# Optimization experiments

Hardware: AMD Instinct MI355X
Metric: run time of the kernel (lower is better)

The kernel has to match this reference:

```python
import jax, jax.numpy as jnp
import numpy as np

U_A = 110.0  # upper bound of feature norm (init kwarg u_a)


def setup_inputs() -> dict:
    key = jax.random.key(0)
    k1, k2, k3, k4 = jax.random.split(key, 4)
    B, C = 256, 100000
    cos_theta = jax.random.normal(k1, (B, C), dtype=jnp.float32)
    cos_theta_m = jax.random.normal(k2, (B, C), dtype=jnp.float32)
    # feature norms in [l_a, u_a] = [10, 110]
    x_norm = 10.0 + 100.0 * jax.random.uniform(k3, (B,), dtype=jnp.float32)
    target = jax.random.randint(k4, (B,), 0, C, dtype=jnp.int32)
    return {"cos_theta": cos_theta, "cos_theta_m": cos_theta_m,
            "x_norm": x_norm, "target": target}


def reference(cos_theta, cos_theta_m, x_norm, target):
    B, C = cos_theta.shape
    # one-hot scatter: one_hot[i, target[i]] = 1 (world_size=1 -> full class dim)
    one_hot = jax.nn.one_hot(target, C, dtype=cos_theta.dtype)  # [B, C]
    # loss_G regularizer: g = x_norm / u_a^2 + 1 / x_norm
    loss_g = jnp.mean(x_norm / (U_A * U_A) + 1.0 / x_norm)
    # margin blend: use cos_theta_m at the target class, cos_theta elsewhere
    output = one_hot * cos_theta_m + (1.0 - one_hot) * cos_theta  # [B, C]
    # cross-entropy with stable log-softmax (distributed LSE collapses to this)
    logp = jax.nn.log_softmax(output, axis=-1)
    loss = -jnp.take_along_axis(logp, target[:, None], axis=-1)[:, 0]  # [B]
    return (loss.mean(), loss_g, one_hot)
```

## Files before the change

kernel.cpp:

```cpp
#include <hip/hip_runtime.h>


#define UA2_INV (1.0f / 12100.0f)
#define SEG 8
#define SEG_SHIFT 3

typedef float v4f __attribute__((ext_vector_type(4)));
typedef float v2f __attribute__((ext_vector_type(2)));

__device__ __forceinline__ void fix_target(float4& v, int c, int t4, int kt4,
                                           float ctm_t) {
    if (c == t4) {
        v.x = (kt4 == 0) ? ctm_t : v.x;
        v.y = (kt4 == 1) ? ctm_t : v.y;
        v.z = (kt4 == 2) ? ctm_t : v.z;
        v.w = (kt4 == 3) ? ctm_t : v.w;
    }
}

__device__ __forceinline__ float exp_sum4(const float4& v) {
    return (__expf(v.x) + __expf(v.y)) + (__expf(v.z) + __expf(v.w));
}

__device__ __forceinline__ void do_fill(float* __restrict__ oh, int seg, int t,
                                        int C, int tid) {
    v4f* __restrict__ oh4 = (v4f*)(oh + 2);
    const int K   = (C - 2) >> 2;
    const int ups = (K + SEG - 1) >> SEG_SHIFT;
    const int u0 = seg * ups;
    const int u1 = min(u0 + ups, K);
    const int ut = (t >= 2) ? ((t - 2) >> 2) : -1;
    const int kt = (t - 2) & 3;

    for (int u = u0 + tid; u < u1; u += 256) {
        v4f z = {0.f, 0.f, 0.f, 0.f};
        if (u == ut) {
            z.x = (kt == 0) ? 1.f : 0.f;
            z.y = (kt == 1) ? 1.f : 0.f;
            z.z = (kt == 2) ? 1.f : 0.f;
            z.w = (kt == 3) ? 1.f : 0.f;
        }
        oh4[u] = z;
    }
    if (seg == 0 && tid == 1) {
        v2f f;
        f.x = (t == 0) ? 1.f : 0.f;
        f.y = (t == 1) ? 1.f : 0.f;
        *(v2f*)oh = f;
    }
    if (seg == SEG - 1) {
        for (int j = 2 + 4 * K + tid; j < C; j += 256)
            oh[j] = (j == t) ? 1.f : 0.f;
    }
}

__device__ __forceinline__ float do_read(const float4* __restrict__ ct4,
                                         const float* __restrict__ ct_row,
                                         int seg, int t, int C, int tid,
                                         float ctm_t) {
    const int nchunk = C >> 2;
    const int cps = (nchunk + SEG - 1) >> SEG_SHIFT;
    const int c0 = seg * cps;
    const int c1 = min(c0 + cps, nchunk);
    const int t4  = t >> 2;
    const int kt4 = t & 3;

    float s0 = 0.f, s1 = 0.f, s2 = 0.f, s3 = 0.f;
    int c = c0 + tid;
    for (; c + 768 < c1; c += 1024) {
        float4 a = ct4[c];
        float4 b = ct4[c + 256];
        float4 d = ct4[c + 512];
        float4 e = ct4[c + 768];
        fix_target(a, c,       t4, kt4, ctm_t);
        fix_target(b, c + 256, t4, kt4, ctm_t);
        fix_target(d, c + 512, t4, kt4, ctm_t);
        fix_target(e, c + 768, t4, kt4, ctm_t);
        s0 += exp_sum4(a);
        s1 += exp_sum4(b);
        s2 += exp_sum4(d);
        s3 += exp_sum4(e);
    }
    for (; c < c1; c += 256) {
        float4 a = ct4[c];
        fix_target(a, c, t4, kt4, ctm_t);
        s0 += exp_sum4(a);
    }
    if (seg == SEG - 1) {
        for (int j = (nchunk << 2) + tid; j < C; j += 256) {
            const float v = (j == t) ? ctm_t : ct_row[j];
            s1 += __expf(v);
        }
    }
    return (s0 + s1) + (s2 + s3);
}

__global__ __launch_bounds__(256) void magloss_part_kernel(
    const float* __restrict__ ct,
    const float* __restrict__ ctm,
    const int*   __restrict__ target,
    float*       __restrict__ onehot,
    float*       __restrict__ part,
    float*       __restrict__ ctmt,
    int C)
{
    const int bid = blockIdx.x;
    const int row = bid >> SEG_SHIFT;
    const int seg = bid & (SEG - 1);
    const size_t base = (size_t)row * (size_t)C;
    const int t = target[row];
    const float ctm_t = ctm[base + (size_t)t];
    const int tid = (int)threadIdx.x;

    if (seg == 0 && tid == 0) ctmt[row] = ctm_t;

    const float4* __restrict__ ct4 = (const float4*)(ct + base);
    float* oh = onehot + base;

    float s;
    if (bid & 1) {
        s = do_read(ct4, ct + base, seg, t, C, tid, ctm_t);
        do_fill(oh, seg, t, C, tid);
    } else {
        do_fill(oh, seg, t, C, tid);
        s = do_read(ct4, ct + base, seg, t, C, tid, ctm_t);
    }

    #pragma unroll
    for (int off = 32; off; off >>= 1)
        s += __shfl_xor(s, off);

    __shared__ float ss[4];
    const int wave = tid >> 6;
    const int lane = tid & 63;
    if (lane == 0) ss[wave] = s;
    __syncthreads();

    if (tid == 0)
        part[bid] = (ss[0] + ss[1]) + (ss[2] + ss[3]);
}

__global__ __launch_bounds__(256) void magloss_finalize_kernel(
    const float* __restrict__ part,
    const float* __restrict__ ctmt,
    const float* __restrict__ x_norm,
    float*       __restrict__ out,
    int B)
{
    const int i = threadIdx.x;
    float l = 0.f, g = 0.f;
    for (int r = i; r < B; r += 256) {
        const float* p = part + (r << SEG_SHIFT);
        float S = 0.f;
        #pragma unroll
        for (int sgi = 0; sgi < SEG; ++sgi) S += p[sgi];
        l += __logf(S) - ctmt[r];
        const float xn = x_norm[r];
        g += xn * UA2_INV + 1.0f / xn;
    }
    #pragma unroll
    for (int off = 32; off; off >>= 1) {
        l += __shfl_xor(l, off);
        g += __shfl_xor(g, off);
    }
    __shared__ float sl[4], sg[4];
    const int wave = i >> 6;
    const int lane = i & 63;
    if (lane == 0) { sl[wave] = l; sg[wave] = g; }
    __syncthreads();
    if (i == 0) {
        float L = 0.f, G = 0.f;
        #pragma unroll
        for (int w = 0; w < 4; ++w) { L += sl[w]; G += sg[w]; }
        out[0] = L / (float)B;
        out[1] = G / (float)B;
    }
}

extern "C" void kernel_launch(void* const* d_in, const int* in_sizes, int n_in,
                              void* d_out, int out_size, void* d_ws, size_t ws_size,
                              hipStream_t stream) {
    const float* ct  = (const float*)d_in[0];
    const float* ctm = (const float*)d_in[1];
    const float* xn  = (const float*)d_in[2];
    const int*   tg  = (const int*)d_in[3];

    const int B = in_sizes[2];
    const int C = in_sizes[0] / B;

    float* out  = (float*)d_out;
    float* part = (float*)d_ws;
    float* ctmt = part + B * SEG;

    magloss_part_kernel<<<B * SEG, 256, 0, stream>>>(ct, ctm, tg, out + 2,
                                                     part, ctmt, C);
    magloss_finalize_kernel<<<1, 256, 0, stream>>>(part, ctmt, xn, out, B);
}
```

Baseline: 32.81 us.

## Fuse finalize into main kernel using atomic last-block reductions

```diff
diff --git a/kernel.cpp b/kernel.cpp
--- a/kernel.cpp
+++ b/kernel.cpp
@@ -20,6 +20,10 @@
 
 __device__ __forceinline__ float exp_sum4(const float4& v) {
     return (__expf(v.x) + __expf(v.y)) + (__expf(v.z) + __expf(v.w));
+}
+
+__device__ __forceinline__ void wait_vmem(float keep) {
+    asm volatile("s_waitcnt vmcnt(0)" :: "v"(keep) : "memory");
 }
 
 __device__ __forceinline__ void do_fill(float* __restrict__ oh, int seg, int t,
@@ -95,14 +99,17 @@
     return (s0 + s1) + (s2 + s3);
 }
 
-__global__ __launch_bounds__(256) void magloss_part_kernel(
+__global__ __launch_bounds__(256) void magloss_kernel(
     const float* __restrict__ ct,
     const float* __restrict__ ctm,
     const int*   __restrict__ target,
-    float*       __restrict__ onehot,
-    float*       __restrict__ part,
-    float*       __restrict__ ctmt,
-    int C)
+    const float* __restrict__ x_norm,
+    float*       __restrict__ out,
+    float*       __restrict__ row_sum,
+    float*       __restrict__ loss_acc,
+    unsigned*    __restrict__ row_cnt,
+    unsigned*    __restrict__ rows_done,
+    int B, int C)
 {
     const int bid = blockIdx.x;
     const int row = bid >> SEG_SHIFT;
@@ -112,10 +119,8 @@
     const float ctm_t = ctm[base + (size_t)t];
     const int tid = (int)threadIdx.x;
 
-    if (seg == 0 && tid == 0) ctmt[row] = ctm_t;
-
     const float4* __restrict__ ct4 = (const float4*)(ct + base);
-    float* oh = onehot + base;
+    float* oh = out + 2 + base;
 
     float s;
     if (bid & 1) {
@@ -126,54 +131,46 @@
         s = do_read(ct4, ct + base, seg, t, C, tid, ctm_t);
     }
 
+    float g = 0.f;
+    if (bid == 0) {
+        for (int r = tid; r < B; r += 256) {
+            const float xn = x_norm[r];
+            g += xn * UA2_INV + 1.0f / xn;
+        }
+    }
+
     #pragma unroll
-    for (int off = 32; off; off >>= 1)
+    for (int off = 32; off; off >>= 1) {
         s += __shfl_xor(s, off);
-
-    __shared__ float ss[4];
+        g += __shfl_xor(g, off);
+    }
+
+    __shared__ float ss[4], sg[4];
     const int wave = tid >> 6;
     const int lane = tid & 63;
-    if (lane == 0) ss[wave] = s;
+    if (lane == 0) { ss[wave] = s; sg[wave] = g; }
     __syncthreads();
 
-    if (tid == 0)
-        part[bid] = (ss[0] + ss[1]) + (ss[2] + ss[3]);
-}
-
-__global__ __launch_bounds__(256) void magloss_finalize_kernel(
-    const float* __restrict__ part,
-    const float* __restrict__ ctmt,
-    const float* __restrict__ x_norm,
-    float*       __restrict__ out,
-    int B)
-{
-    const int i = threadIdx.x;
-    float l = 0.f, g = 0.f;
-    for (int r = i; r < B; r += 256) {
-        const float* p = part + (r << SEG_SHIFT);
-        float S = 0.f;
-        #pragma unroll
-        for (int sgi = 0; sgi < SEG; ++sgi) S += p[sgi];
-        l += __logf(S) - ctmt[r];
-        const float xn = x_norm[r];
-        g += xn * UA2_INV + 1.0f / xn;
-    }
-    #pragma unroll
-    for (int off = 32; off; off >>= 1) {
-        l += __shfl_xor(l, off);
-        g += __shfl_xor(g, off);
-    }
-    __shared__ float sl[4], sg[4];
-    const int wave = i >> 6;
-    const int lane = i & 63;
-    if (lane == 0) { sl[wave] = l; sg[wave] = g; }
-    __syncthreads();
-    if (i == 0) {
-        float L = 0.f, G = 0.f;
-        #pragma unroll
-        for (int w = 0; w < 4; ++w) { L += sl[w]; G += sg[w]; }
-        out[0] = L / (float)B;
-        out[1] = G / (float)B;
+    if (tid == 0) {
+        const float blk = (ss[0] + ss[1]) + (ss[2] + ss[3]);
+
+        if (bid == 0)
+            out[1] = ((sg[0] + sg[1]) + (sg[2] + sg[3])) / (float)B;
+
+        const float old = atomicAdd(&row_sum[row], blk);
+        wait_vmem(old);
+        const unsigned oc = atomicAdd(&row_cnt[row], 1u);
+        if (oc == (unsigned)(SEG - 1)) {
+            const float S = atomicAdd(&row_sum[row], 0.0f);
+            const float l = __logf(S) - ctm_t;
+            const float olda = atomicAdd(loss_acc, l);
+            wait_vmem(olda);
+            const unsigned od = atomicAdd(rows_done, 1u);
+            if (od == (unsigned)(B - 1)) {
+                const float total = atomicAdd(loss_acc, 0.0f);
+                out[0] = total / (float)B;
+            }
+        }
     }
 }
 
@@ -188,11 +185,17 @@
     const int B = in_sizes[2];
     const int C = in_sizes[0] / B;
 
-    float* out  = (float*)d_out;
-    float* part = (float*)d_ws;
-    float* ctmt = part + B * SEG;
-
-    magloss_part_kernel<<<B * SEG, 256, 0, stream>>>(ct, ctm, tg, out + 2,
-                                                     part, ctmt, C);
-    magloss_finalize_kernel<<<1, 256, 0, stream>>>(part, ctmt, xn, out, B);
-}
+    float* out = (float*)d_out;
+
+    float*    row_sum   = (float*)d_ws;
+    float*    loss_acc  = row_sum + B;
+    unsigned* row_cnt   = (unsigned*)(loss_acc + 1);
+    unsigned* rows_done = row_cnt + B;
+
+    const size_t zbytes = (size_t)(2 * B + 2) * sizeof(float);
+    hipMemsetAsync(d_ws, 0, zbytes, stream);
+
+    magloss_kernel<<<B * SEG, 256, 0, stream>>>(ct, ctm, tg, xn, out,
+                                                row_sum, loss_acc,
+                                                row_cnt, rows_done, B, C);
+}
```

Result: slower. 39.62 us (+20.8%).
